# Optimization experiments

Hardware: AMD Instinct MI355X
Metric: run time of the kernel (lower is better)

Reference implementation:

```python
import jax, jax.numpy as jnp
import numpy as np

# dims: batch, seq, d_model, mlp_width, num_experts, lora_rank
B, S, D, M, E, R = 4, 1024, 2048, 5632, 8, 16
LORA_ALPHA = 32
SCALING = LORA_ALPHA / R  # = 2.0


def setup_inputs() -> dict:
    key = jax.random.key(0)
    ks = jax.random.split(key, 13)
    s = 0.02
    f32 = jnp.float32
    return {
        'x':  jax.random.normal(ks[0], (B, S, D), f32),
        # router: nn.Linear(d_model, num_experts)
        'Wr': jax.random.normal(ks[1], (E, D), f32) * s,
        'br': jax.random.normal(ks[2], (E,), f32) * s,
        # frozen original MLP weights (torch Linear layout [out, in])
        'Wg': jax.random.normal(ks[3], (M, D), f32) * s,
        'Wu': jax.random.normal(ks[4], (M, D), f32) * s,
        'Wd': jax.random.normal(ks[5], (D, M), f32) * s,
        # shared LoRA A matrices [rank, fan_in]
        'Ag': jax.random.normal(ks[6], (R, D), f32) * s,
        'Au': jax.random.normal(ks[7], (R, D), f32) * s,
        'Ad': jax.random.normal(ks[8], (R, M), f32) * s,
        # per-expert LoRA B matrices [E, fan_out, rank] (zero-init in the
        # original; randomized here so gradients/outputs are non-trivial)
        'Bg': jax.random.normal(ks[9], (E, M, R), f32) * s,
        'Bu': jax.random.normal(ks[10], (E, M, R), f32) * s,
        'Bd': jax.random.normal(ks[11], (E, D, R), f32) * s,
    }


def _lora_moe_dense(x, W, A, Bexp, routing):
    """Dense MoE LoRA: original_proj(x) + sum_e routing[...,e] * (x @ A^T @ B_e^T) * scaling.
    x: [b,s,in], W: [out,in], A: [r,in], Bexp: [E,out,r], routing: [b,s,E].
    Identical math to stacking all experts then weighted-summing, but the
    shared A lets us weight the tiny [b,s,E,r] hidden instead of [b,s,E,out].
    """
    orig = jnp.einsum('bsi,oi->bso', x, W)
    h = jnp.einsum('bsi,ri->bsr', x, A)            # shared low-rank hidden
    hw = jnp.einsum('bsr,bse->bser', h, routing)   # routing-weighted hidden
    lora = jnp.einsum('bser,eor->bso', hw, Bexp) * SCALING
    return orig + lora


def reference(x, Wr, br, Wg, Wu, Wd, Ag, Au, Ad, Bg, Bu, Bd):
    logits = jnp.einsum('bsd,ed->bse', x, Wr) + br
    routing = jax.nn.softmax(logits, axis=-1)
    idx = jnp.argmax(routing, axis=-1)
    y_hard = jax.nn.one_hot(idx, E, dtype=logits.dtype)
    # straight-through expert choice
    expert_choice = y_hard - jax.lax.stop_gradient(routing) + routing
    gate = _lora_moe_dense(x, Wg, Ag, Bg, routing)
    up = _lora_moe_dense(x, Wu, Au, Bu, routing)
    h = jax.nn.silu(gate) * up  # LLaMA-style SwiGLU act_fn
    out = _lora_moe_dense(h, Wd, Ad, Bd, routing)
    return out, routing, expert_choice
```

## Files before the change

### kernel.cpp

```cpp
#include <hip/hip_runtime.h>

#define DEV __device__ __forceinline__

typedef unsigned short u16;
typedef __bf16 bf16x8 __attribute__((ext_vector_type(8)));
typedef float f32x4 __attribute__((ext_vector_type(4)));

static DEV u16 f2bf(float f) {
    union { float f; unsigned u; } v; v.f = f;
    unsigned r = v.u + 0x7fffu + ((v.u >> 16) & 1u);
    return (u16)(r >> 16);
}
static DEV float bf2f(u16 u) {
    union { unsigned u; float f; } v; v.u = ((unsigned)u) << 16;
    return v.f;
}
static DEV void g2l16(const u16* g, u16* l) {
    __builtin_amdgcn_global_load_lds(
        (const __attribute__((address_space(1))) void*)g,
        (__attribute__((address_space(3))) void*)l, 16, 0, 0);
}

#define BAR()    do { __builtin_amdgcn_s_barrier(); __builtin_amdgcn_sched_barrier(0); } while (0)
#define WAITV(N) asm volatile("s_waitcnt vmcnt(" #N ")" ::: "memory")

#define MM16(A, B, FMO, FNO) do {                                            \
    __builtin_amdgcn_s_setprio(1);                                           \
    _Pragma("unroll")                                                        \
    for (int fm_ = 0; fm_ < 4; ++fm_)                                        \
      _Pragma("unroll")                                                      \
      for (int fn_ = 0; fn_ < 2; ++fn_)                                      \
        _Pragma("unroll")                                                    \
        for (int ks_ = 0; ks_ < 2; ++ks_)                                    \
          acc[(FMO) + fm_][(FNO) + fn_] = __builtin_amdgcn_mfma_f32_16x16x32_bf16( \
              A[fm_][ks_], B[fn_][ks_], acc[(FMO) + fm_][(FNO) + fn_], 0, 0, 0); \
    __builtin_amdgcn_s_setprio(0);                                           \
} while (0)


__global__ __launch_bounds__(256) void k_conv(
    const float* __restrict__ Wg, const float* __restrict__ Wu, const float* __restrict__ Wd,
    const float* __restrict__ Bg, const float* __restrict__ Bu, const float* __restrict__ Bd,
    u16* __restrict__ Wg16, u16* __restrict__ Wu16, u16* __restrict__ Wd16,
    u16* __restrict__ Bgx, u16* __restrict__ Bux, u16* __restrict__ Bdx)
{
    const long long NW = 2883584;
    const long long NB = 180224;
    const long long ND = 65536;
    long long gid = (long long)blockIdx.x * 256 + threadIdx.x;
    if (gid < 3 * NW) {
        const float* s; u16* d; long long g = gid;
        if (g < NW)           { s = Wg; d = Wg16; }
        else if (g < 2 * NW)  { s = Wu; d = Wu16; g -= NW; }
        else                  { s = Wd; d = Wd16; g -= 2 * NW; }
        float4 v = *(const float4*)(s + g * 4);
        ushort4 o; o.x = f2bf(v.x); o.y = f2bf(v.y); o.z = f2bf(v.z); o.w = f2bf(v.w);
        *(ushort4*)(d + g * 4) = o;
    } else {
        long long g = gid - 3 * NW;
        const float* s; u16* d; int nr;
        if (g < NB)               { s = Bg; d = Bgx; nr = 5632; }
        else if (g < 2 * NB)      { s = Bu; d = Bux; nr = 5632; g -= NB; }
        else if (g < 2 * NB + ND) { s = Bd; d = Bdx; nr = 2048; g -= 2 * NB; }
        else return;
        int n = (int)(g >> 5);
        int j0 = ((int)g & 31) * 4;
        int e = j0 >> 4, r0 = j0 & 15;
        float4 v = *(const float4*)&s[((size_t)e * nr + n) * 16 + r0];
        ushort4 o; o.x = f2bf(v.x); o.y = f2bf(v.y); o.z = f2bf(v.z); o.w = f2bf(v.w);
        *(ushort4*)&d[(size_t)n * 128 + j0] = o;
    }
}

__global__ __launch_bounds__(256) void k_router(
    const float* __restrict__ x, const float* __restrict__ Wr,
    const float* __restrict__ Ag, const float* __restrict__ Au,
    u16* __restrict__ x16, float* __restrict__ fin1)
{
    __shared__ float xs[64][65];
    __shared__ float wsm[40][64];
    const int rb = blockIdx.x, ksp = blockIdx.y;
    const int row0 = rb * 64;
    const int t = threadIdx.x;
    const int rloc = t & 63, og = t >> 6;
    float acc[10];
#pragma unroll
    for (int o = 0; o < 10; ++o) acc[o] = 0.f;

    for (int c4 = 0; c4 < 4; ++c4) {
        const int k0 = ksp * 256 + c4 * 64;
        __syncthreads();
#pragma unroll
        for (int i = 0; i < 4; ++i) {
            int idx = t + i * 256;
            int r = idx >> 4, c = (idx & 15) * 4;
            float4 v = *(const float4*)&x[(size_t)(row0 + r) * 2048 + k0 + c];
            xs[r][c + 0] = v.x; xs[r][c + 1] = v.y; xs[r][c + 2] = v.z; xs[r][c + 3] = v.w;
            ushort4 o; o.x = f2bf(v.x); o.y = f2bf(v.y); o.z = f2bf(v.z); o.w = f2bf(v.w);
            *(ushort4*)&x16[(size_t)(row0 + r) * 2048 + k0 + c] = o;
        }
#pragma unroll
        for (int i = 0; i < 3; ++i) {
            int idx = t + i * 256;
            if (idx < 640) {
                int r = idx >> 4, c = (idx & 15) * 4;
                const float* src = (r < 8) ? (Wr + (size_t)r * 2048)
                                : (r < 24) ? (Ag + (size_t)(r - 8) * 2048)
                                           : (Au + (size_t)(r - 24) * 2048);
                float4 v = *(const float4*)&src[k0 + c];
                wsm[r][c + 0] = v.x; wsm[r][c + 1] = v.y; wsm[r][c + 2] = v.z; wsm[r][c + 3] = v.w;
            }
        }
        __syncthreads();
#pragma unroll
        for (int k = 0; k < 64; ++k) {
            float xv = xs[rloc][k];
#pragma unroll
            for (int o = 0; o < 10; ++o) acc[o] += xv * wsm[og * 10 + o][k];
        }
    }
    float* dst = fin1 + ((size_t)ksp * 4096 + row0 + rloc) * 40 + og * 10;
#pragma unroll
    for (int o = 0; o < 10; ++o) dst[o] = acc[o];
}

__global__ __launch_bounds__(64) void k_fin1(
    const float* __restrict__ fin1, const float* __restrict__ br,
    float* __restrict__ routing_ws, float* __restrict__ out_rt, float* __restrict__ out_ec,
    u16* __restrict__ hwg, u16* __restrict__ hwu)
{
    const int row = blockIdx.x * 64 + threadIdx.x;
    float s[40];
#pragma unroll
    for (int j = 0; j < 40; ++j) s[j] = 0.f;
    for (int p = 0; p < 8; ++p) {
        const float* src = fin1 + ((size_t)p * 4096 + row) * 40;
#pragma unroll
        for (int j = 0; j < 40; ++j) s[j] += src[j];
    }
    float lg[8]; float m = -1e30f;
#pragma unroll
    for (int e = 0; e < 8; ++e) { lg[e] = s[e] + br[e]; m = fmaxf(m, lg[e]); }
    float ex[8]; float sum = 0.f;
#pragma unroll
    for (int e = 0; e < 8; ++e) { ex[e] = expf(lg[e] - m); sum += ex[e]; }
    float r8[8];
#pragma unroll
    for (int e = 0; e < 8; ++e) r8[e] = ex[e] / sum;
    int best = 0;
#pragma unroll
    for (int e = 1; e < 8; ++e) if (r8[e] > r8[best]) best = e;
#pragma unroll
    for (int e = 0; e < 8; ++e) {
        routing_ws[(size_t)row * 8 + e] = r8[e];
        out_rt[(size_t)row * 8 + e] = r8[e];
        float yh = (e == best) ? 1.f : 0.f;
        out_ec[(size_t)row * 8 + e] = (yh - r8[e]) + r8[e];
    }
#pragma unroll
    for (int e = 0; e < 8; ++e) {
        float re = r8[e];
#pragma unroll
        for (int rk = 0; rk < 16; ++rk) {
            hwg[(size_t)row * 128 + e * 16 + rk] = f2bf(2.f * s[8 + rk] * re);
            hwu[(size_t)row * 128 + e * 16 + rk] = f2bf(2.f * s[24 + rk] * re);
        }
    }
}

template<int MODE>
__global__ __launch_bounds__(512, 2) void k_gemm8(
    const u16* __restrict__ A0, int lda0,
    const u16* __restrict__ A1g, const u16* __restrict__ A1u,
    const u16* __restrict__ B0g, int ldb0, const u16* __restrict__ B0u,
    const u16* __restrict__ B1g, const u16* __restrict__ B1u,
    int Ksplit,
    float* __restrict__ outF0, float* __restrict__ outF1,
    u16* __restrict__ outHg, u16* __restrict__ outHu,
    int nbm, int nbn)
{
    __shared__ u16 lds[65536];
    const int t = threadIdx.x;
    const int nwg = (int)gridDim.x;
    const int orig = (int)blockIdx.x;
    const int sw = (orig & 7) * (nwg >> 3) + (orig >> 3);
    const int bm = sw % nbm; const int rest = sw / nbm;
    const int bn = rest % nbn; const int z = rest / nbn;

    const int row0 = bm * 256, col0 = bn * 256;
    int ktb, ntl;
    if (MODE == 0) { ktb = z ? 46 : 0; ntl = z ? 44 : 46; }
    else           { ktb = 0;          ntl = 34; }
    const int kend = ktb + ntl;
    const u16* A1 = (MODE == 1 && z) ? A1u : A1g;
    const u16* B0 = (MODE == 1 && z) ? B0u : B0g;
    const u16* B1 = (MODE == 1 && z) ? B1u : B1g;

    const int lane = t & 63, lr = lane & 15, lg = lane >> 4;
    const int wid = t >> 6, wr = wid >> 2, wcol = wid & 3;
    const int arow = wr * 128 + lr;
    const int brow = wcol * 64 + lr;
    const int sa = (arow & 7) << 3;
    const int sb = (brow & 7) << 3;

    const int rA = t >> 3;
    const int c00u = ((t & 7) * 8) ^ ((rA & 7) << 3);
    const u16* bA0 = A0 + (size_t)(row0 + rA) * lda0 + c00u;
    const u16* bA1 = A1 + ((size_t)(row0 + rA) << 7) + c00u;
    const u16* bB0 = B0 + (size_t)(col0 + rA) * ldb0 + c00u;
    const u16* bB1 = B1 + ((size_t)(col0 + rA) << 7) + c00u;
    const int ldsT = t * 8;

    auto stgA = [&](int kt, int h, int bufu) {
        const int k0 = kt * 64;
        const bool p2 = (k0 >= Ksplit);
        const u16* b = p2 ? (bA1 + (k0 - Ksplit)) : (bA0 + k0);
        const size_t ld = p2 ? (size_t)128 : (size_t)lda0;
        g2l16(b + (size_t)(h * 128) * ld,      &lds[bufu + h * 8192 + ldsT]);
        g2l16(b + (size_t)(h * 128 + 64) * ld, &lds[bufu + h * 8192 + 4096 + ldsT]);
    };
    auto stgB = [&](int kt, int h, int bufu) {
        const int k0 = kt * 64;
        const bool p2 = (k0 >= Ksplit);
        const u16* b = p2 ? (bB1 + (k0 - Ksplit)) : (bB0 + k0);
        const size_t ld = p2 ? (size_t)128 : (size_t)ldb0;
        g2l16(b + (size_t)(h * 128) * ld,      &lds[32768 + bufu + h * 8192 + ldsT]);
        g2l16(b + (size_t)(h * 128 + 64) * ld, &lds[32768 + bufu + h * 8192 + 4096 + ldsT]);
    };
    auto rdA = [&](int bufu, int fb, bf16x8 (&d)[4][2]) {
#pragma unroll
        for (int fm = 0; fm < 4; ++fm)
#pragma unroll
            for (int ks = 0; ks < 2; ++ks)
                d[fm][ks] = *(const bf16x8*)&lds[bufu + (arow + (fb + fm) * 16) * 64
                                                 + (((ks << 5) | (lg << 3)) ^ sa)];
    };
    auto rdB = [&](int bufu, int fb, bf16x8 (&d)[2][2]) {
#pragma unroll
        for (int fn = 0; fn < 2; ++fn)
#pragma unroll
            for (int ks = 0; ks < 2; ++ks)
                d[fn][ks] = *(const bf16x8*)&lds[32768 + bufu + (brow + (fb + fn) * 16) * 64
                                                 + (((ks << 5) | (lg << 3)) ^ sb)];
    };

    f32x4 acc[8][4];
    const f32x4 zf = {0.f, 0.f, 0.f, 0.f};
#pragma unroll
    for (int i = 0; i < 8; ++i)
#pragma unroll
        for (int j = 0; j < 4; ++j) acc[i][j] = zf;

    stgA(ktb, 0, 0); stgA(ktb, 1, 0);
    stgB(ktb, 0, 0); stgB(ktb, 1, 0);
    stgB(ktb + 1, 0, 16384); stgB(ktb + 1, 1, 16384);
    WAITV(4);
    BAR();

    const int ni = ntl >> 1;
    for (int i = 0; i < ni; ++i) {
        const int kt0 = ktb + 2 * i, kt1 = kt0 + 1;
        const bool s2 = (kt0 + 2 < kend), s3 = (kt1 + 2 < kend);
        bf16x8 alo[4][2], ahi[4][2], b01[2][2], b23[2][2];
        rdA(0, 0, alo); rdB(0, 0, b01); rdB(0, 2, b23);
        stgA(kt1, 0, 16384); stgA(kt1, 1, 16384);
        BAR();
        MM16(alo, b01, 0, 0); MM16(alo, b23, 0, 2);
        BAR();
        rdA(0, 4, ahi);
        if (s2) { stgB(kt0 + 2, 0, 0); stgB(kt0 + 2, 1, 0); }
        BAR();
        MM16(ahi, b01, 4, 0); MM16(ahi, b23, 4, 2);
        if (s2) { WAITV(4); } else { WAITV(0); }
        BAR();
        rdA(16384, 0, alo); rdB(16384, 0, b01); rdB(16384, 2, b23);
        if (s2) { stgA(kt0 + 2, 0, 0); stgA(kt0 + 2, 1, 0); }
        BAR();
        MM16(alo, b01, 0, 0); MM16(alo, b23, 0, 2);
        BAR();
        rdA(16384, 4, ahi);
        if (s3) { stgB(kt1 + 2, 0, 16384); stgB(kt1 + 2, 1, 16384); }
        BAR();
        MM16(ahi, b01, 4, 0); MM16(ahi, b23, 4, 2);
        if (s3) { WAITV(4); }
        BAR();
    }

#pragma unroll
    for (int fm = 0; fm < 8; ++fm) {
#pragma unroll
        for (int fn = 0; fn < 4; ++fn) {
            const int r = row0 + wr * 128 + fm * 16 + lg * 4;
            const int c = col0 + wcol * 64 + fn * 16 + lr;
            f32x4 v = acc[fm][fn];
            if constexpr (MODE == 0) {
                float* out = z ? outF1 : outF0;
#pragma unroll
                for (int j = 0; j < 4; ++j) out[(size_t)(r + j) * 2048 + c] = v[j];
            } else {
                u16* out = z ? outHu : outHg;
#pragma unroll
                for (int j = 0; j < 4; ++j) out[(size_t)(r + j) * 5632 + c] = f2bf(v[j]);
            }
        }
    }
}

__global__ __launch_bounds__(256) void k_hd(
    u16* __restrict__ g, const u16* __restrict__ u,
    const float* __restrict__ Ad, float* __restrict__ fin2)
{
    __shared__ float hs[64][65];
    __shared__ float as2[16][64];
    const int rb = blockIdx.x, ksp = blockIdx.y;
    const int row0 = rb * 64;
    const int t = threadIdx.x;
    const int rloc = t & 63, og = t >> 6;
    float acc[4] = {0.f, 0.f, 0.f, 0.f};
    for (int c4 = 0; c4 < 11; ++c4) {
        const int k0 = ksp * 704 + c4 * 64;
        __syncthreads();
#pragma unroll
        for (int i = 0; i < 4; ++i) {
            int idx = t + i * 256;
            int r = idx >> 4, cc = (idx & 15) * 4;
            size_t go = (size_t)(row0 + r) * 5632 + k0 + cc;
            ushort4 gv = *(const ushort4*)&g[go];
            ushort4 uv = *(const ushort4*)&u[go];
            float h0, h1, h2, h3;
            { float gg = bf2f(gv.x); h0 = gg / (1.f + __expf(-gg)) * bf2f(uv.x); }
            { float gg = bf2f(gv.y); h1 = gg / (1.f + __expf(-gg)) * bf2f(uv.y); }
            { float gg = bf2f(gv.z); h2 = gg / (1.f + __expf(-gg)) * bf2f(uv.z); }
            { float gg = bf2f(gv.w); h3 = gg / (1.f + __expf(-gg)) * bf2f(uv.w); }
            hs[r][cc + 0] = h0; hs[r][cc + 1] = h1; hs[r][cc + 2] = h2; hs[r][cc + 3] = h3;
            ushort4 hv; hv.x = f2bf(h0); hv.y = f2bf(h1); hv.z = f2bf(h2); hv.w = f2bf(h3);
            *(ushort4*)&g[go] = hv;
        }
        {
            int r = t >> 4, cc = (t & 15) * 4;
            float4 w = *(const float4*)&Ad[(size_t)r * 5632 + k0 + cc];
            as2[r][cc + 0] = w.x; as2[r][cc + 1] = w.y; as2[r][cc + 2] = w.z; as2[r][cc + 3] = w.w;
        }
        __syncthreads();
#pragma unroll
        for (int k = 0; k < 64; ++k) {
            float hv = hs[rloc][k];
#pragma unroll
            for (int o = 0; o < 4; ++o) acc[o] += hv * as2[og * 4 + o][k];
        }
    }
    float* dst = fin2 + ((size_t)ksp * 4096 + row0 + rloc) * 16 + og * 4;
#pragma unroll
    for (int o = 0; o < 4; ++o) dst[o] = acc[o];
}

__global__ __launch_bounds__(64) void k_fin2(
    const float* __restrict__ fin2, const float* __restrict__ routing_ws, u16* __restrict__ hwd)
{
    const int row = blockIdx.x * 64 + threadIdx.x;
    float hd[16];
#pragma unroll
    for (int j = 0; j < 16; ++j) hd[j] = 0.f;
    for (int p = 0; p < 8; ++p) {
        const float* src = fin2 + ((size_t)p * 4096 + row) * 16;
#pragma unroll
        for (int j = 0; j < 16; ++j) hd[j] += src[j];
    }
#pragma unroll
    for (int e = 0; e < 8; ++e) {
        float re = routing_ws[(size_t)row * 8 + e];
#pragma unroll
        for (int rk = 0; rk < 16; ++rk)
            hwd[(size_t)row * 128 + e * 16 + rk] = f2bf(2.f * hd[rk] * re);
    }
}

__global__ __launch_bounds__(256) void k_reduce(
    float* __restrict__ o, const float* __restrict__ p1)
{
    size_t i = ((size_t)blockIdx.x * 256 + threadIdx.x) * 4;
    float4 a = *(const float4*)&o[i];
    float4 b = *(const float4*)&p1[i];
    float4 r; r.x = a.x + b.x; r.y = a.y + b.y; r.z = a.z + b.z; r.w = a.w + b.w;
    *(float4*)&o[i] = r;
}

extern "C" void kernel_launch(void* const* d_in, const int* in_sizes, int n_in,
                              void* d_out, int out_size, void* d_ws, size_t ws_size,
                              hipStream_t stream)
{
    (void)in_sizes; (void)n_in; (void)out_size; (void)ws_size;
    const float* x  = (const float*)d_in[0];
    const float* Wr = (const float*)d_in[1];
    const float* br = (const float*)d_in[2];
    const float* Wg = (const float*)d_in[3];
    const float* Wu = (const float*)d_in[4];
    const float* Wd = (const float*)d_in[5];
    const float* Ag = (const float*)d_in[6];
    const float* Au = (const float*)d_in[7];
    const float* Ad = (const float*)d_in[8];
    const float* Bg = (const float*)d_in[9];
    const float* Bu = (const float*)d_in[10];
    const float* Bd = (const float*)d_in[11];

    float* outp   = (float*)d_out;
    float* out_rt = outp + 8388608;
    float* out_ec = out_rt + 32768;

    char* p = (char*)d_ws;
    auto carve = [&](size_t n) -> char* { char* r = p; p += (n + 255) & ~(size_t)255; return r; };
    u16*   x16        = (u16*)carve(16777216);
    u16*   hwg        = (u16*)carve(1048576);
    u16*   hwu        = (u16*)carve(1048576);
    u16*   hwd        = (u16*)carve(1048576);
    float* routing_ws = (float*)carve(131072);
    float* fin1       = (float*)carve(5242880);
    float* fin2       = (float*)carve(2097152);
    u16*   Wg16       = (u16*)carve(23068672);
    u16*   Wu16       = (u16*)carve(23068672);
    u16*   Wd16       = (u16*)carve(23068672);
    u16*   Bgx        = (u16*)carve(1441792);
    u16*   Bux        = (u16*)carve(1441792);
    u16*   Bdx        = (u16*)carve(524288);
    u16*   gbuf       = (u16*)carve(46137344);
    u16*   ubuf       = (u16*)carve(46137344);
    float* part1      = (float*)ubuf;

    k_conv<<<dim3(35456), dim3(256), 0, stream>>>(Wg, Wu, Wd, Bg, Bu, Bd,
                                                  Wg16, Wu16, Wd16, Bgx, Bux, Bdx);
    k_router<<<dim3(64, 8), dim3(256), 0, stream>>>(x, Wr, Ag, Au, x16, fin1);
    k_fin1<<<dim3(64), dim3(64), 0, stream>>>(fin1, br, routing_ws, out_rt, out_ec, hwg, hwu);
    k_gemm8<1><<<dim3(704), dim3(512), 0, stream>>>(
        x16, 2048, hwg, hwu, Wg16, 2048, Wu16, Bgx, Bux,
        2048, (float*)nullptr, (float*)nullptr, gbuf, ubuf, 16, 22);
    k_hd<<<dim3(64, 8), dim3(256), 0, stream>>>(gbuf, ubuf, Ad, fin2);
    k_fin2<<<dim3(64), dim3(64), 0, stream>>>(fin2, routing_ws, hwd);
    k_gemm8<0><<<dim3(256), dim3(512), 0, stream>>>(
        gbuf, 5632, hwd, hwd, Wd16, 5632, Wd16, Bdx, Bdx,
        5632, outp, part1, (u16*)nullptr, (u16*)nullptr, 16, 8);
    k_reduce<<<dim3(8192), dim3(256), 0, stream>>>(outp, part1);
}
```

Before: 438.4 us.

## Triple-buffer A tiles in LDS to prefetch two k-steps ahead

Grows the shared-memory buffer from 128 KB to 160 KB so A tiles rotate through three LDS slots while B keeps two. A loads are now issued two k-tiles ahead into a free slot instead of reusing the slot just consumed. The goal is to give global-to-LDS loads more latency slack before the waitcnt barriers. The cost is more LDS per workgroup, which with launch_bounds(512,2) may cut the number of resident workgroups per CU and so reduce occupancy.

```diff
diff --git a/kernel.cpp b/kernel.cpp
--- a/kernel.cpp
+++ b/kernel.cpp
@@ -179,7 +179,7 @@
     u16* __restrict__ outHg, u16* __restrict__ outHu,
     int nbm, int nbn)
 {
-    __shared__ u16 lds[65536];
+    __shared__ u16 lds[81920];
     const int t = threadIdx.x;
     const int nwg = (int)gridDim.x;
     const int orig = (int)blockIdx.x;
@@ -191,7 +191,6 @@
     int ktb, ntl;
     if (MODE == 0) { ktb = z ? 46 : 0; ntl = z ? 44 : 46; }
     else           { ktb = 0;          ntl = 34; }
-    const int kend = ktb + ntl;
     const u16* A1 = (MODE == 1 && z) ? A1u : A1g;
     const u16* B0 = (MODE == 1 && z) ? B0u : B0g;
     const u16* B1 = (MODE == 1 && z) ? B1u : B1g;
@@ -211,21 +210,25 @@
     const u16* bB1 = B1 + ((size_t)(col0 + rA) << 7) + c00u;
     const int ldsT = t * 8;
 
-    auto stgA = [&](int kt, int h, int bufu) {
+    auto stgA = [&](int kt, int offu) {
         const int k0 = kt * 64;
         const bool p2 = (k0 >= Ksplit);
         const u16* b = p2 ? (bA1 + (k0 - Ksplit)) : (bA0 + k0);
         const size_t ld = p2 ? (size_t)128 : (size_t)lda0;
-        g2l16(b + (size_t)(h * 128) * ld,      &lds[bufu + h * 8192 + ldsT]);
-        g2l16(b + (size_t)(h * 128 + 64) * ld, &lds[bufu + h * 8192 + 4096 + ldsT]);
+        g2l16(b,             &lds[offu + ldsT]);
+        g2l16(b + 64 * ld,   &lds[offu + 4096 + ldsT]);
+        g2l16(b + 128 * ld,  &lds[offu + 8192 + ldsT]);
+        g2l16(b + 192 * ld,  &lds[offu + 12288 + ldsT]);
     };
-    auto stgB = [&](int kt, int h, int bufu) {
+    auto stgB = [&](int kt, int offu) {
         const int k0 = kt * 64;
         const bool p2 = (k0 >= Ksplit);
         const u16* b = p2 ? (bB1 + (k0 - Ksplit)) : (bB0 + k0);
         const size_t ld = p2 ? (size_t)128 : (size_t)ldb0;
-        g2l16(b + (size_t)(h * 128) * ld,      &lds[32768 + bufu + h * 8192 + ldsT]);
-        g2l16(b + (size_t)(h * 128 + 64) * ld, &lds[32768 + bufu + h * 8192 + 4096 + ldsT]);
+        g2l16(b,             &lds[offu + ldsT]);
+        g2l16(b + 64 * ld,   &lds[offu + 4096 + ldsT]);
+        g2l16(b + 128 * ld,  &lds[offu + 8192 + ldsT]);
+        g2l16(b + 192 * ld,  &lds[offu + 12288 + ldsT]);
     };
     auto rdA = [&](int bufu, int fb, bf16x8 (&d)[4][2]) {
 #pragma unroll
@@ -240,7 +243,7 @@
         for (int fn = 0; fn < 2; ++fn)
 #pragma unroll
             for (int ks = 0; ks < 2; ++ks)
-                d[fn][ks] = *(const bf16x8*)&lds[32768 + bufu + (brow + (fb + fn) * 16) * 64
+                d[fn][ks] = *(const bf16x8*)&lds[bufu + (brow + (fb + fn) * 16) * 64
                                                  + (((ks << 5) | (lg << 3)) ^ sb)];
     };
 
@@ -251,38 +254,41 @@
 #pragma unroll
         for (int j = 0; j < 4; ++j) acc[i][j] = zf;
 
-    stgA(ktb, 0, 0); stgA(ktb, 1, 0);
-    stgB(ktb, 0, 0); stgB(ktb, 1, 0);
-    stgB(ktb + 1, 0, 16384); stgB(ktb + 1, 1, 16384);
-    WAITV(4);
+    stgA(ktb, 0);       stgB(ktb, 49152);
+    stgA(ktb + 1, 16384); stgB(ktb + 1, 65536);
+    WAITV(8);
     BAR();
 
     const int ni = ntl >> 1;
     for (int i = 0; i < ni; ++i) {
         const int kt0 = ktb + 2 * i, kt1 = kt0 + 1;
-        const bool s2 = (kt0 + 2 < kend), s3 = (kt1 + 2 < kend);
+        const bool s2 = (2 * i + 2 < ntl);
+        const unsigned a0 = (unsigned)(2 * i) % 3u;
+        const unsigned a1 = (a0 + 1 >= 3u) ? a0 - 2u : a0 + 1u;
+        const unsigned aS = (a1 + 1 >= 3u) ? a1 - 2u : a1 + 1u;
+        const int offA0 = (int)a0 * 16384, offA1 = (int)a1 * 16384, offAS = (int)aS * 16384;
         bf16x8 alo[4][2], ahi[4][2], b01[2][2], b23[2][2];
-        rdA(0, 0, alo); rdB(0, 0, b01); rdB(0, 2, b23);
-        stgA(kt1, 0, 16384); stgA(kt1, 1, 16384);
+        rdA(offA0, 0, alo); rdB(49152, 0, b01); rdB(49152, 2, b23);
+        if (s2) stgA(kt0 + 2, offAS);
         BAR();
         MM16(alo, b01, 0, 0); MM16(alo, b23, 0, 2);
         BAR();
-        rdA(0, 4, ahi);
-        if (s2) { stgB(kt0 + 2, 0, 0); stgB(kt0 + 2, 1, 0); }
+        rdA(offA0, 4, ahi);
+        if (s2) stgB(kt0 + 2, 49152);
         BAR();
         MM16(ahi, b01, 4, 0); MM16(ahi, b23, 4, 2);
-        if (s2) { WAITV(4); } else { WAITV(0); }
-        BAR();
-        rdA(16384, 0, alo); rdB(16384, 0, b01); rdB(16384, 2, b23);
-        if (s2) { stgA(kt0 + 2, 0, 0); stgA(kt0 + 2, 1, 0); }
+        if (s2) { WAITV(8); } else { WAITV(0); }
+        BAR();
+        rdA(offA1, 0, alo); rdB(65536, 0, b01); rdB(65536, 2, b23);
+        if (s2) stgA(kt1 + 2, offA0);
         BAR();
         MM16(alo, b01, 0, 0); MM16(alo, b23, 0, 2);
         BAR();
-        rdA(16384, 4, ahi);
-        if (s3) { stgB(kt1 + 2, 0, 16384); stgB(kt1 + 2, 1, 16384); }
+        rdA(offA1, 4, ahi);
+        if (s2) stgB(kt1 + 2, 65536);
         BAR();
         MM16(ahi, b01, 4, 0); MM16(ahi, b23, 4, 2);
-        if (s3) { WAITV(4); }
+        if (s2) { WAITV(8); }
         BAR();
     }
 
```

Measured after the change: 439.4 us. Within noise of the previous version (+0.2%).
